# Kernel tuning notes

Measured on AMD Instinct MI355X. Metric: run time of the kernel, lower is better.

## Reference

```python
import jax, jax.numpy as jnp
import numpy as np

NEG = -9e15
LN_EPS = 1e-5
ALPHA = 0.2  # LeakyReLU negative slope


def setup_inputs() -> dict:
    key = jax.random.key(0)
    ks = jax.random.split(key, 10)
    B, N, Din, H, F, L = 8, 512, 64, 8, 128, 2
    x = jax.random.normal(ks[0], (B, N, Din), dtype=jnp.float32)
    adj = jax.random.randint(ks[1], (B, N, N), 0, 2, dtype=jnp.int32)
    Wp = jax.random.normal(ks[2], (Din, F), dtype=jnp.float32) * 0.12
    bp = jnp.zeros((F,), dtype=jnp.float32)
    W_heads = jax.random.normal(ks[3], (L, H, F, F), dtype=jnp.float32) * 0.08
    a_heads = jax.random.normal(ks[4], (L, H, 2 * F), dtype=jnp.float32) * 0.08
    W_out = jax.random.normal(ks[5], (L, H * F, F), dtype=jnp.float32) * 0.03
    a_out = jax.random.normal(ks[6], (L, 2 * F), dtype=jnp.float32) * 0.08
    ln_g = jnp.ones((L, F), dtype=jnp.float32)
    ln_b = jnp.zeros((L, F), dtype=jnp.float32)
    return {"x": x, "adj": adj, "Wp": Wp, "bp": bp, "W_heads": W_heads,
            "a_heads": a_heads, "W_out": W_out, "a_out": a_out,
            "ln_g": ln_g, "ln_b": ln_b}


def _gat_heads(x, W, a, adj_mask):
    # x:[B,N,Fin]  W:[H,Fin,F]  a:[H,2F]  adj_mask:[B,N,N] bool
    h = jnp.einsum('bni,hio->bhno', x, W)          # [B,H,N,F]
    F = h.shape[-1]
    # a_input @ a == (h_i . a1) + (h_j . a2): split attention vector,
    # mathematically identical to the concat formulation.
    s1 = jnp.einsum('bhnf,hf->bhn', h, a[:, :F])   # source term
    s2 = jnp.einsum('bhnf,hf->bhn', h, a[:, F:])   # target term
    e = jax.nn.leaky_relu(s1[:, :, :, None] + s2[:, :, None, :], ALPHA)  # [B,H,N,N]
    att = jnp.where(adj_mask[:, None], e, NEG)
    att = jax.nn.softmax(att, axis=-1)
    return jnp.einsum('bhnm,bhmf->bhnf', att, h)   # [B,H,N,F]


def _gat_single(x, W, a, adj_mask):
    # out_att head (concat=False, no ELU)
    h = jnp.einsum('bni,io->bno', x, W)            # [B,N,F]
    F = h.shape[-1]
    s1 = h @ a[:F]                                  # [B,N]
    s2 = h @ a[F:]
    e = jax.nn.leaky_relu(s1[:, :, None] + s2[:, None, :], ALPHA)
    att = jnp.where(adj_mask, e, NEG)
    att = jax.nn.softmax(att, axis=-1)
    return jnp.einsum('bnm,bmf->bnf', att, h)


def _layernorm(x, g, b):
    mu = jnp.mean(x, axis=-1, keepdims=True)
    var = jnp.var(x, axis=-1, keepdims=True)
    return (x - mu) * jax.lax.rsqrt(var + LN_EPS) * g + b


def reference(x, adj, Wp, bp, W_heads, a_heads, W_out, a_out, ln_g, ln_b):
    adj_mask = adj > 0                              # [B,N,N]
    L = W_heads.shape[0]
    B, N = x.shape[0], x.shape[1]
    # input projection (eval mode -> dropout is identity)
    h = jax.nn.relu(x @ Wp + bp)                    # [B,N,F]
    for i in range(L):
        residual = h
        heads = _gat_heads(h, W_heads[i], a_heads[i], adj_mask)      # [B,H,N,F]
        heads = jax.nn.elu(heads)                                     # concat=True -> ELU
        multi = jnp.transpose(heads, (0, 2, 1, 3)).reshape(B, N, -1)  # [B,N,H*F]
        out = _gat_single(multi, W_out[i], a_out[i], adj_mask)        # [B,N,F]
        h = _layernorm(out + residual, ln_g[i], ln_b[i])
        if i < L - 1:
            h = jax.nn.relu(h)
    return h
```

## Files before the change

kernel.cpp:

```cpp
#include <hip/hip_runtime.h>


constexpr int B = 8, N = 512, DIN = 64, H = 8, F = 128;
constexpr int BN = B * N;
constexpr float ALPHA_LR = 0.2f;
constexpr float EPS_LN = 1e-5f;
constexpr float FLOW = -3.0e38f;

typedef __attribute__((ext_vector_type(8))) short short8;
typedef __attribute__((ext_vector_type(4))) float f32x4;

__device__ __forceinline__ f32x4 mfma16(short8 a, short8 b, f32x4 c) {
  return __builtin_amdgcn_mfma_f32_16x16x32_bf16(a, b, c, 0, 0, 0);
}

__device__ __forceinline__ short f2bf(float f) {
  union { float f; unsigned u; } v;
  v.f = f;
  unsigned r = v.u + 0x7FFFu + ((v.u >> 16) & 1u);
  return (short)(r >> 16);
}

__global__ __launch_bounds__(256) void k_setup(
    const float* __restrict__ x, const int* __restrict__ adj,
    const float* __restrict__ Wp, const float* __restrict__ bp,
    const float* __restrict__ W_heads, const float* __restrict__ W_out,
    float* __restrict__ h, short* __restrict__ hb,
    unsigned long long* __restrict__ amask, short* __restrict__ WTh,
    short* __restrict__ WoT) {
  __shared__ float T[32][33];
  __shared__ float xr[2][64];
  int blk = blockIdx.x, tid = threadIdx.x;
  if (blk < 8192) {
    int w = blk * 4 + (tid >> 6);
    int lane = tid & 63;
    int v = adj[(size_t)w * 64 + lane];
    unsigned long long m = __ballot(v > 0);
    if (lane == 0) amask[w] = m;
  } else if (blk < 10240) {
    int rb = blk - 8192;
    int half = tid >> 7, f = tid & 127;
    int row = rb * 2 + half;
    if (f < 64) xr[half][f] = x[(size_t)row * DIN + f];
    __syncthreads();
    float acc = bp[f];
#pragma unroll
    for (int i = 0; i < DIN; i++) acc = fmaf(xr[half][i], Wp[i * F + f], acc);
    acc = fmaxf(acc, 0.f);
    h[(size_t)row * F + f] = acc;
    hb[(size_t)row * F + f] = f2bf(acc);
  } else {
    const float* in;
    short* out;
    int R, C, bx, by, bt;
    if (blk < 10496) {
      int i = blk - 10240;
      in = W_heads; out = WTh; R = 128; C = 128;
      bx = i & 3; by = (i >> 2) & 3; bt = i >> 4;
    } else {
      int i = blk - 10496;
      in = W_out; out = WoT; R = 1024; C = 128;
      bx = i & 3; by = (i >> 2) & 31; bt = i >> 7;
    }
    int c0 = bx * 32, r0 = by * 32;
    const float* ip = in + (size_t)bt * R * C;
    short* op = out + (size_t)bt * R * C;
    {
      int r = tid >> 3, c4 = (tid & 7) * 4;
      float4 v = *(const float4*)(ip + (size_t)(r0 + r) * C + c0 + c4);
      T[r][c4] = v.x; T[r][c4 + 1] = v.y; T[r][c4 + 2] = v.z; T[r][c4 + 3] = v.w;
    }
    __syncthreads();
    {
      int cr = tid >> 3, q = (tid & 7) * 4;
      short4 o;
      o.x = f2bf(T[q][cr]); o.y = f2bf(T[q + 1][cr]);
      o.z = f2bf(T[q + 2][cr]); o.w = f2bf(T[q + 3][cr]);
      *(short4*)(op + (size_t)(c0 + cr) * R + r0 + q) = o;
    }
  }
}

__global__ __launch_bounds__(256) void k_proj_heads_mfma(
    const short* __restrict__ WT, const short* __restrict__ hb,
    const float* __restrict__ ah_base, short* __restrict__ hhT,
    float* __restrict__ s1, float* __restrict__ s2) {
  int n0 = blockIdx.x * 128;
  int ft = blockIdx.y;
  int bh = blockIdx.z;
  int b = bh >> 3, hd = bh & 7;
  constexpr int LK = 136;
  __shared__ short As[64 * LK];
  __shared__ short Bs[128 * LK];
  int tid = threadIdx.x, lane = tid & 63, w = tid >> 6;
  {
    int r = tid >> 2, q = tid & 3;
    const uint4* g = (const uint4*)(WT + ((size_t)hd * F + ft * 64 + r) * F) + q * 4;
    uint4* lp = (uint4*)(As + r * LK) + q * 4;
    lp[0] = g[0]; lp[1] = g[1]; lp[2] = g[2]; lp[3] = g[3];
  }
  {
    int q = tid & 3;
    for (int r = tid >> 2; r < 128; r += 64) {
      const uint4* g = (const uint4*)(hb + ((size_t)(b * N + n0 + r)) * F) + q * 4;
      uint4* lp = (uint4*)(Bs + r * LK) + q * 4;
      lp[0] = g[0]; lp[1] = g[1]; lp[2] = g[2]; lp[3] = g[3];
    }
  }
  __syncthreads();
  int arow = lane & 15, koff = (lane >> 4) * 8;
  f32x4 acc[4][2] = {};
#pragma unroll
  for (int ks = 0; ks < 4; ks++) {
    short8 a[4], bb[2];
#pragma unroll
    for (int rt = 0; rt < 4; rt++)
      a[rt] = *(const short8*)(As + (rt * 16 + arow) * LK + ks * 32 + koff);
#pragma unroll
    for (int cj = 0; cj < 2; cj++)
      bb[cj] = *(const short8*)(Bs + ((2 * w + cj) * 16 + arow) * LK + ks * 32 + koff);
#pragma unroll
    for (int rt = 0; rt < 4; rt++)
#pragma unroll
      for (int cj = 0; cj < 2; cj++)
        acc[rt][cj] = mfma16(a[rt], bb[cj], acc[rt][cj]);
  }
  short* outp = hhT + (size_t)bh * F * N;
  int crow0 = (lane >> 4) * 4;
#pragma unroll
  for (int rt = 0; rt < 4; rt++)
#pragma unroll
    for (int cj = 0; cj < 2; cj++) {
      int fo = ft * 64 + rt * 16 + crow0;
      int n = n0 + (2 * w + cj) * 16 + arow;
#pragma unroll
      for (int r = 0; r < 4; r++)
        outp[(size_t)(fo + r) * N + n] = f2bf(acc[rt][cj][r]);
    }
  const float* ah = ah_base + (size_t)hd * 2 * F;
  float pa1[2] = {0.f, 0.f}, pa2[2] = {0.f, 0.f};
#pragma unroll
  for (int rt = 0; rt < 4; rt++) {
    int fo = ft * 64 + rt * 16 + crow0;
#pragma unroll
    for (int r = 0; r < 4; r++) {
      float a1v = ah[fo + r], a2v = ah[F + fo + r];
      pa1[0] = fmaf(a1v, acc[rt][0][r], pa1[0]);
      pa1[1] = fmaf(a1v, acc[rt][1][r], pa1[1]);
      pa2[0] = fmaf(a2v, acc[rt][0][r], pa2[0]);
      pa2[1] = fmaf(a2v, acc[rt][1][r], pa2[1]);
    }
  }
#pragma unroll
  for (int cj = 0; cj < 2; cj++) {
    float v1 = pa1[cj], v2 = pa2[cj];
    v1 += __shfl_xor(v1, 16); v1 += __shfl_xor(v1, 32);
    v2 += __shfl_xor(v2, 16); v2 += __shfl_xor(v2, 32);
    if (lane < 16) {
      int n = n0 + (2 * w + cj) * 16 + lane;
      atomicAdd(&s1[(size_t)bh * N + n], v1);
      atomicAdd(&s2[(size_t)bh * N + n], v2);
    }
  }
}

__global__ __launch_bounds__(256) void k_proj_out_mfma(
    const short* __restrict__ WoT, const short* __restrict__ multi,
    const float* __restrict__ ao, short* __restrict__ hsT,
    float* __restrict__ s1, float* __restrict__ s2) {
  int ft = blockIdx.x, nt = blockIdx.y, b = blockIdx.z;
  constexpr int LK = 136;
  __shared__ short As[32 * LK];
  __shared__ short Bs[64 * LK];
  int tid = threadIdx.x, lane = tid & 63, w = tid >> 6;
  int arow = lane & 15, koff = (lane >> 4) * 8;
  const int KT = H * F;
  f32x4 acc[2] = {};
  for (int k0 = 0; k0 < KT; k0 += 128) {
    __syncthreads();
    {
      int r = tid >> 3, e = tid & 7;
      const uint4* gp = (const uint4*)(WoT + (size_t)(ft * 32 + r) * KT + k0) + e * 2;
      uint4* lp = (uint4*)(As + r * LK) + e * 2;
      lp[0] = gp[0]; lp[1] = gp[1];
    }
    {
      int r = tid >> 2, q = tid & 3;
      const uint4* gp =
          (const uint4*)(multi + (size_t)(b * N + nt * 64 + r) * KT + k0) + q * 4;
      uint4* lp = (uint4*)(Bs + r * LK) + q * 4;
      lp[0] = gp[0]; lp[1] = gp[1]; lp[2] = gp[2]; lp[3] = gp[3];
    }
    __syncthreads();
#pragma unroll
    for (int ks = 0; ks < 4; ks++) {
      short8 b0 = *(const short8*)(Bs + (w * 16 + arow) * LK + ks * 32 + koff);
      short8 a0 = *(const short8*)(As + arow * LK + ks * 32 + koff);
      short8 a1 = *(const short8*)(As + (16 + arow) * LK + ks * 32 + koff);
      acc[0] = mfma16(a0, b0, acc[0]);
      acc[1] = mfma16(a1, b0, acc[1]);
    }
  }
  int crow0 = (lane >> 4) * 4;
  short* op = hsT + (size_t)b * F * N;
#pragma unroll
  for (int rt = 0; rt < 2; rt++)
#pragma unroll
    for (int r = 0; r < 4; r++)
      op[(size_t)(ft * 32 + rt * 16 + crow0 + r) * N + nt * 64 + w * 16 + arow] =
          f2bf(acc[rt][r]);
  float pa1 = 0.f, pa2 = 0.f;
#pragma unroll
  for (int rt = 0; rt < 2; rt++) {
    int fo = ft * 32 + rt * 16 + crow0;
#pragma unroll
    for (int r = 0; r < 4; r++) {
      pa1 = fmaf(ao[fo + r], acc[rt][r], pa1);
      pa2 = fmaf(ao[F + fo + r], acc[rt][r], pa2);
    }
  }
  pa1 += __shfl_xor(pa1, 16); pa1 += __shfl_xor(pa1, 32);
  pa2 += __shfl_xor(pa2, 16); pa2 += __shfl_xor(pa2, 32);
  if (lane < 16) {
    int n = nt * 64 + w * 16 + lane;
    atomicAdd(&s1[(size_t)b * N + n], pa1);
    atomicAdd(&s2[(size_t)b * N + n], pa2);
  }
}

__global__ __launch_bounds__(256) void k_attn_heads3(
    const short* __restrict__ VT, const float* __restrict__ s1g,
    const float* __restrict__ s2g, const unsigned long long* __restrict__ amask,
    short* __restrict__ multi) {
  int n0 = blockIdx.x * 64;
  int hd = blockIdx.y, b = blockIdx.z;
  int bh = b * H + hd;
  constexpr int LVK = 136;
  __shared__ short Vs[128 * LVK];
  __shared__ short Pf[16 * 64 * 8];
  __shared__ float s2all[512];
  __shared__ float s1r[64], mrow[64], linv[64];
  __shared__ float red[64][4];

  int tid = threadIdx.x, lane = tid & 63, w = tid >> 6;
  s2all[tid] = s2g[(size_t)bh * N + tid];
  s2all[tid + 256] = s2g[(size_t)bh * N + tid + 256];
  if (tid < 64) s1r[tid] = s1g[(size_t)bh * N + n0 + tid];
  __syncthreads();
  {
    const unsigned long long* mq = amask + ((size_t)(b * N + n0 + lane)) * 8;
    float mx = FLOW;
#pragma unroll
    for (int j = 0; j < 2; j++) {
      unsigned long long mb = mq[w * 2 + j];
      int base = w * 128 + j * 64;
      unsigned lo = (unsigned)mb, hi = (unsigned)(mb >> 32);
#pragma unroll
      for (int k = 0; k < 32; k++) {
        mx = ((lo >> k) & 1u) ? fmaxf(mx, s2all[base + k]) : mx;
        mx = ((hi >> k) & 1u) ? fmaxf(mx, s2all[base + 32 + k]) : mx;
      }
    }
    red[lane][w] = mx;
  }
  __syncthreads();
  if (tid < 64) {
    float m2 = fmaxf(fmaxf(red[tid][0], red[tid][1]),
                     fmaxf(red[tid][2], red[tid][3]));
    float xm = s1r[tid] + m2;
    mrow[tid] = xm > 0.f ? xm : ALPHA_LR * xm;
  }
  float lp = 0.f;
  int arow = lane & 15, koff = (lane >> 4) * 8;
  f32x4 acc[4][2] = {};
  const short* Vg = VT + (size_t)bh * F * N;
  const unsigned long long* mp = amask + ((size_t)(b * N + n0 + lane)) * 8;
  for (int mc = 0; mc < 4; mc++) {
    int m0 = mc * 128;
    __syncthreads();
    {
      int fr = tid >> 1, hf = tid & 1;
      const uint4* g4 = (const uint4*)(Vg + (size_t)fr * N + m0 + hf * 64);
      uint4* l4 = (uint4*)(Vs + fr * LVK + hf * 64);
#pragma unroll
      for (int k = 0; k < 8; k++) l4[k] = g4[k];
    }
    {
      float s1v = s1r[lane], mr = mrow[lane];
      unsigned bits = (unsigned)(mp[mc * 2 + (w >> 1)] >> ((w & 1) * 32));
      short* pbase = Pf + (((lane >> 4) * 4 + w) * 64) * 8;
#pragma unroll
      for (int q = 0; q < 4; q++) {
        short8 pk;
#pragma unroll
        for (int j = 0; j < 8; j++) {
          float xv = s1v + s2all[m0 + w * 32 + q * 8 + j];
          xv = xv > 0.f ? xv : ALPHA_LR * xv;
          float p = __expf(xv - mr);
          p = ((bits >> (q * 8 + j)) & 1u) ? p : 0.f;
          lp += p;
          pk[j] = f2bf(p);
        }
        *(short8*)(pbase + ((q << 4) | (lane & 15)) * 8) = pk;
      }
    }
    __syncthreads();
#pragma unroll
    for (int ks = 0; ks < 4; ks++) {
      short8 a[4];
#pragma unroll
      for (int rt = 0; rt < 4; rt++)
        a[rt] = *(const short8*)(Pf + ((rt * 4 + ks) * 64 + lane) * 8);
#pragma unroll
      for (int cj = 0; cj < 2; cj++) {
        short8 bb = *(const short8*)(Vs + ((w * 2 + cj) * 16 + arow) * LVK +
                                     ks * 32 + koff);
#pragma unroll
        for (int rt = 0; rt < 4; rt++)
          acc[rt][cj] = mfma16(a[rt], bb, acc[rt][cj]);
      }
    }
  }
  __syncthreads();
  red[lane][w] = lp;
  __syncthreads();
  if (tid < 64)
    linv[tid] = 1.f / (red[tid][0] + red[tid][1] + red[tid][2] + red[tid][3]);
  __syncthreads();
  int crow0 = (lane >> 4) * 4;
#pragma unroll
  for (int rt = 0; rt < 4; rt++)
#pragma unroll
    for (int cj = 0; cj < 2; cj++) {
      int fcol = (w * 2 + cj) * 16 + arow;
#pragma unroll
      for (int rr = 0; rr < 4; rr++) {
        int nrow = rt * 16 + crow0 + rr;
        float v = acc[rt][cj][rr] * linv[nrow];
        v = v > 0.f ? v : __expf(v) - 1.f;
        multi[((size_t)(b * N + n0 + nrow)) * (H * F) + hd * F + fcol] = f2bf(v);
      }
    }
}

template <int LAST>
__global__ __launch_bounds__(256) void k_attn_single3(
    const short* __restrict__ VT, const float* __restrict__ s1g,
    const float* __restrict__ s2g, const unsigned long long* __restrict__ amask,
    const float* __restrict__ resid, const float* __restrict__ lng,
    const float* __restrict__ lnb, float* __restrict__ hout,
    short* __restrict__ hbout, float* __restrict__ dout) {
  int n0 = blockIdx.x * 16;
  int b = blockIdx.y;
  constexpr int LVK = 136;
  __shared__ short Vs[128 * LVK];
  __shared__ short Pf[4 * 64 * 8];
  __shared__ float s2all[512];
  __shared__ float Ot[16][132];
  __shared__ float redS[16][16], redQ[16][16];
  __shared__ float s1r[16], mrow[16], linv[16], muA[16], rsA[16];

  int tid = threadIdx.x, lane = tid & 63, w = tid >> 6;
  s2all[tid] = s2g[(size_t)b * N + tid];
  s2all[tid + 256] = s2g[(size_t)b * N + tid + 256];
  if (tid < 16) s1r[tid] = s1g[(size_t)b * N + n0 + tid];
  __syncthreads();
  {
    int r = tid & 15, seg = tid >> 4;
    unsigned long long mb = amask[((size_t)(b * N + n0 + r)) * 8 + (seg >> 1)];
    unsigned bits = (unsigned)(mb >> ((seg & 1) * 32));
    float mx = FLOW;
#pragma unroll
    for (int k = 0; k < 32; k++)
      mx = ((bits >> k) & 1u) ? fmaxf(mx, s2all[seg * 32 + k]) : mx;
    redS[r][seg] = mx;
  }
  __syncthreads();
  if (tid < 16) {
    float m2 = FLOW;
#pragma unroll
    for (int k = 0; k < 16; k++) m2 = fmaxf(m2, redS[tid][k]);
    float xm = s1r[tid] + m2;
    mrow[tid] = xm > 0.f ? xm : ALPHA_LR * xm;
  }
  float lp = 0.f;
  int arow = lane & 15, koff = (lane >> 4) * 8;
  int pr = tid & 15, pq = (tid >> 4) & 3;
  f32x4 acc[2] = {};
  const short* Vg = VT + (size_t)b * F * N;
  const unsigned long long* mp = amask + ((size_t)(b * N + n0 + pr)) * 8;
  for (int mc = 0; mc < 4; mc++) {
    int m0 = mc * 128;
    __syncthreads();
    {
      int fr = tid >> 1, hf = tid & 1;
      const uint4* g4 = (const uint4*)(Vg + (size_t)fr * N + m0 + hf * 64);
      uint4* l4 = (uint4*)(Vs + fr * LVK + hf * 64);
#pragma unroll
      for (int k = 0; k < 8; k++) l4[k] = g4[k];
    }
    {
      float s1v = s1r[pr], mr = mrow[pr];
      unsigned bits = (unsigned)(mp[mc * 2 + (w >> 1)] >> ((w & 1) * 32));
      short8 pk;
#pragma unroll
      for (int j = 0; j < 8; j++) {
        float xv = s1v + s2all[m0 + w * 32 + pq * 8 + j];
        xv = xv > 0.f ? xv : ALPHA_LR * xv;
        float p = __expf(xv - mr);
        p = ((bits >> (pq * 8 + j)) & 1u) ? p : 0.f;
        lp += p;
        pk[j] = f2bf(p);
      }
      *(short8*)(Pf + (w * 64 + ((pq << 4) | pr)) * 8) = pk;
    }
    __syncthreads();
#pragma unroll
    for (int ks = 0; ks < 4; ks++) {
      short8 a = *(const short8*)(Pf + (ks * 64 + lane) * 8);
#pragma unroll
      for (int cj = 0; cj < 2; cj++) {
        short8 bb = *(const short8*)(Vs + ((w * 2 + cj) * 16 + arow) * LVK +
                                     ks * 32 + koff);
        acc[cj] = mfma16(a, bb, acc[cj]);
      }
    }
  }
  __syncthreads();
  redS[pr][tid >> 4] = lp;
  __syncthreads();
  if (tid < 16) {
    float l = 0.f;
#pragma unroll
    for (int k = 0; k < 16; k++) l += redS[tid][k];
    linv[tid] = 1.f / l;
  }
  __syncthreads();
  int crow0 = (lane >> 4) * 4;
#pragma unroll
  for (int cj = 0; cj < 2; cj++) {
    int fcol = (w * 2 + cj) * 16 + arow;
#pragma unroll
    for (int rr = 0; rr < 4; rr++) {
      int row = crow0 + rr;
      Ot[row][fcol] = acc[cj][rr] * linv[row];
    }
  }
  __syncthreads();
  int r2 = tid >> 4, f8 = (tid & 15) * 8;
  size_t gbase = ((size_t)(b * N + n0 + r2)) * F + f8;
  float v[8];
  float s = 0.f, sq = 0.f;
#pragma unroll
  for (int j = 0; j < 8; j++) {
    float t = Ot[r2][f8 + j] + resid[gbase + j];
    v[j] = t;
    s += t;
    sq = fmaf(t, t, sq);
  }
  redS[r2][tid & 15] = s;
  redQ[r2][tid & 15] = sq;
  __syncthreads();
  if (tid < 16) {
    float ss = 0.f, qq = 0.f;
#pragma unroll
    for (int k = 0; k < 16; k++) { ss += redS[tid][k]; qq += redQ[tid][k]; }
    float mu = ss * (1.f / F);
    muA[tid] = mu;
    rsA[tid] = rsqrtf(qq * (1.f / F) - mu * mu + EPS_LN);
  }
  __syncthreads();
  float mu = muA[r2], rs = rsA[r2];
#pragma unroll
  for (int j = 0; j < 8; j++) {
    float y = (v[j] - mu) * rs * lng[f8 + j] + lnb[f8 + j];
    if (LAST) {
      dout[gbase + j] = y;
    } else {
      y = fmaxf(y, 0.f);
      hout[gbase + j] = y;
      hbout[gbase + j] = f2bf(y);
    }
  }
}

extern "C" void kernel_launch(void* const* d_in, const int* in_sizes, int n_in,
                              void* d_out, int out_size, void* d_ws,
                              size_t ws_size, hipStream_t stream) {
  const float* x = (const float*)d_in[0];
  const int* adj = (const int*)d_in[1];
  const float* Wp = (const float*)d_in[2];
  const float* bp = (const float*)d_in[3];
  const float* W_heads = (const float*)d_in[4];
  const float* a_heads = (const float*)d_in[5];
  const float* W_out = (const float*)d_in[6];
  const float* a_out = (const float*)d_in[7];
  const float* ln_g = (const float*)d_in[8];
  const float* ln_b = (const float*)d_in[9];

  char* p = (char*)d_ws;
  auto alloc = [&](size_t bytes) {
    char* r = p;
    p += (bytes + 255) & ~(size_t)255;
    return r;
  };
  float* sA = (float*)alloc((size_t)2 * 73728 * 4);
  short* WTh = (short*)alloc((size_t)2 * H * F * F * 2);
  short* WoT = (short*)alloc((size_t)2 * H * F * F * 2);
  unsigned long long* amask = (unsigned long long*)alloc((size_t)BN * 8 * 8);
  float* h = (float*)alloc((size_t)BN * F * 4);
  short* hb = (short*)alloc((size_t)BN * F * 2);
  short* hhT = (short*)alloc((size_t)B * H * F * N * 2);
  short* multi = (short*)alloc((size_t)BN * H * F * 2);
  short* hsT = (short*)alloc((size_t)B * F * N * 2);

  hipMemsetAsync(sA, 0, (size_t)2 * 73728 * 4, stream);
  k_setup<<<dim3(10752), 256, 0, stream>>>(x, adj, Wp, bp, W_heads, W_out, h,
                                           hb, amask, WTh, WoT);
  for (int l = 0; l < 2; l++) {
    float* s1h = sA + (size_t)l * 73728;
    float* s2h = s1h + 32768;
    float* s1o = s2h + 32768;
    float* s2o = s1o + 4096;
    k_proj_heads_mfma<<<dim3(4, 2, 64), 256, 0, stream>>>(
        WTh + (size_t)l * H * F * F, hb, a_heads + (size_t)l * H * 2 * F, hhT,
        s1h, s2h);
    k_attn_heads3<<<dim3(8, 8, 8), 256, 0, stream>>>(hhT, s1h, s2h, amask,
                                                     multi);
    k_proj_out_mfma<<<dim3(4, 8, 8), 256, 0, stream>>>(
        WoT + (size_t)l * F * H * F, multi, a_out + (size_t)l * 2 * F, hsT, s1o,
        s2o);
    if (l == 0)
      k_attn_single3<0><<<dim3(32, 8), 256, 0, stream>>>(
          hsT, s1o, s2o, amask, h, ln_g, ln_b, h, hb, nullptr);
    else
      k_attn_single3<1><<<dim3(32, 8), 256, 0, stream>>>(
          hsT, s1o, s2o, amask, h, ln_g + F, ln_b + F, nullptr, nullptr,
          (float*)d_out);
  }
}
```

Measured before the change: 189.7 us.

## Fuse all GAT stages into one cooperative persistent kernel with grid syncs

```diff
diff --git a/kernel.cpp b/kernel.cpp
--- a/kernel.cpp
+++ b/kernel.cpp
@@ -1,5 +1,8 @@
 #include <hip/hip_runtime.h>
-
+#include <hip/hip_cooperative_groups.h>
+
+
+namespace cg = cooperative_groups;
 
 constexpr int B = 8, N = 512, DIN = 64, H = 8, F = 128;
 constexpr int BN = B * N;
@@ -21,89 +24,114 @@
   return (short)(r >> 16);
 }
 
-__global__ __launch_bounds__(256) void k_setup(
-    const float* __restrict__ x, const int* __restrict__ adj,
-    const float* __restrict__ Wp, const float* __restrict__ bp,
-    const float* __restrict__ W_heads, const float* __restrict__ W_out,
-    float* __restrict__ h, short* __restrict__ hb,
-    unsigned long long* __restrict__ amask, short* __restrict__ WTh,
-    short* __restrict__ WoT) {
-  __shared__ float T[32][33];
-  __shared__ float xr[2][64];
-  int blk = blockIdx.x, tid = threadIdx.x;
-  if (blk < 8192) {
-    int w = blk * 4 + (tid >> 6);
-    int lane = tid & 63;
-    int v = adj[(size_t)w * 64 + lane];
-    unsigned long long m = __ballot(v > 0);
-    if (lane == 0) amask[w] = m;
-  } else if (blk < 10240) {
-    int rb = blk - 8192;
+struct KParams {
+  const float* x; const int* adj; const float* Wp; const float* bp;
+  const float* W_heads; const float* a_heads; const float* W_out;
+  const float* a_out; const float* ln_g; const float* ln_b;
+  float* h; short* hb; unsigned long long* amask; short* WTh; short* WoT;
+  short* hhT; short* multi; short* hsT; float* sA; float* dout;
+};
+
+struct SM_PH { short As[64 * 136]; short Bs[128 * 136]; };
+struct SM_AH {
+  short Vs[128 * 136]; short Pf[16 * 64 * 8]; float s2all[512];
+  float s1r[64]; float mrow[64]; float linv[64]; float red[64][4];
+};
+struct SM_PO { short As[32 * 136]; short Bs[32 * 136]; };
+struct SM_AS {
+  short Vs[128 * 136]; short Pf[4 * 64 * 8]; float s2all[512];
+  float Ot[16][132]; float redS[16][16]; float redQ[16][16];
+  float s1r[16]; float mrow[16]; float linv[16]; float muA[16]; float rsA[16];
+};
+struct SM_SU { float T[32][33]; float xr[2][64]; };
+
+__device__ __forceinline__ void st_setup(const KParams& P, int bid, int tid,
+                                         char* smraw) {
+  for (int i = tid; i < 288; i += 256) P.sA[(size_t)bid * 288 + i] = 0.f;
+  {
+    int lane = tid & 63, wv = tid >> 6;
+    int v[16];
+#pragma unroll
+    for (int j = 0; j < 16; j++) {
+      int w = (bid + j * 512) * 4 + wv;
+      v[j] = P.adj[(size_t)w * 64 + lane];
+    }
+#pragma unroll
+    for (int j = 0; j < 16; j++) {
+      int w = (bid + j * 512) * 4 + wv;
+      unsigned long long m = __ballot(v[j] > 0);
+      if (lane == 0) P.amask[w] = m;
+    }
+  }
+  {
+    SM_SU* s = (SM_SU*)smraw;
     int half = tid >> 7, f = tid & 127;
-    int row = rb * 2 + half;
-    if (f < 64) xr[half][f] = x[(size_t)row * DIN + f];
-    __syncthreads();
-    float acc = bp[f];
-#pragma unroll
-    for (int i = 0; i < DIN; i++) acc = fmaf(xr[half][i], Wp[i * F + f], acc);
-    acc = fmaxf(acc, 0.f);
-    h[(size_t)row * F + f] = acc;
-    hb[(size_t)row * F + f] = f2bf(acc);
-  } else {
-    const float* in;
-    short* out;
-    int R, C, bx, by, bt;
-    if (blk < 10496) {
-      int i = blk - 10240;
-      in = W_heads; out = WTh; R = 128; C = 128;
-      bx = i & 3; by = (i >> 2) & 3; bt = i >> 4;
+    for (int u = bid; u < 2048; u += 512) {
+      int row = u * 2 + half;
+      __syncthreads();
+      if (f < 64) s->xr[half][f] = P.x[(size_t)row * DIN + f];
+      __syncthreads();
+      float acc = P.bp[f];
+#pragma unroll
+      for (int i = 0; i < DIN; i++)
+        acc = fmaf(s->xr[half][i], P.Wp[i * F + f], acc);
+      acc = fmaxf(acc, 0.f);
+      P.h[(size_t)row * F + f] = acc;
+      P.hb[(size_t)row * F + f] = f2bf(acc);
+    }
+  }
+  {
+    SM_SU* s = (SM_SU*)smraw;
+    const float* in; short* out; int R, C, bx, by, bt;
+    if (bid < 256) {
+      in = P.W_heads; out = P.WTh; R = 128; C = 128;
+      bx = bid & 3; by = (bid >> 2) & 3; bt = bid >> 4;
     } else {
-      int i = blk - 10496;
-      in = W_out; out = WoT; R = 1024; C = 128;
+      int i = bid - 256;
+      in = P.W_out; out = P.WoT; R = 1024; C = 128;
       bx = i & 3; by = (i >> 2) & 31; bt = i >> 7;
     }
     int c0 = bx * 32, r0 = by * 32;
     const float* ip = in + (size_t)bt * R * C;
     short* op = out + (size_t)bt * R * C;
+    __syncthreads();
     {
       int r = tid >> 3, c4 = (tid & 7) * 4;
       float4 v = *(const float4*)(ip + (size_t)(r0 + r) * C + c0 + c4);
-      T[r][c4] = v.x; T[r][c4 + 1] = v.y; T[r][c4 + 2] = v.z; T[r][c4 + 3] = v.w;
+      s->T[r][c4] = v.x; s->T[r][c4 + 1] = v.y;
+      s->T[r][c4 + 2] = v.z; s->T[r][c4 + 3] = v.w;
     }
     __syncthreads();
     {
       int cr = tid >> 3, q = (tid & 7) * 4;
       short4 o;
-      o.x = f2bf(T[q][cr]); o.y = f2bf(T[q + 1][cr]);
-      o.z = f2bf(T[q + 2][cr]); o.w = f2bf(T[q + 3][cr]);
+      o.x = f2bf(s->T[q][cr]); o.y = f2bf(s->T[q + 1][cr]);
+      o.z = f2bf(s->T[q + 2][cr]); o.w = f2bf(s->T[q + 3][cr]);
       *(short4*)(op + (size_t)(c0 + cr) * R + r0 + q) = o;
     }
   }
 }
 
-__global__ __launch_bounds__(256) void k_proj_heads_mfma(
-    const short* __restrict__ WT, const short* __restrict__ hb,
-    const float* __restrict__ ah_base, short* __restrict__ hhT,
-    float* __restrict__ s1, float* __restrict__ s2) {
-  int n0 = blockIdx.x * 128;
-  int ft = blockIdx.y;
-  int bh = blockIdx.z;
+__device__ __forceinline__ void st_proj_heads(
+    const KParams& P, const short* WT, const float* ah_base, float* s1,
+    float* s2, int bid, int tid, char* smraw) {
+  SM_PH* sm = (SM_PH*)smraw;
+  int nt = bid & 3, ft = (bid >> 2) & 1, bh = bid >> 3;
   int b = bh >> 3, hd = bh & 7;
+  int n0 = nt * 128;
   constexpr int LK = 136;
-  __shared__ short As[64 * LK];
-  __shared__ short Bs[128 * LK];
-  int tid = threadIdx.x, lane = tid & 63, w = tid >> 6;
+  int lane = tid & 63, w = tid >> 6;
   {
     int r = tid >> 2, q = tid & 3;
     const uint4* g = (const uint4*)(WT + ((size_t)hd * F + ft * 64 + r) * F) + q * 4;
-    uint4* lp = (uint4*)(As + r * LK) + q * 4;
+    uint4* lp = (uint4*)(sm->As + r * LK) + q * 4;
     lp[0] = g[0]; lp[1] = g[1]; lp[2] = g[2]; lp[3] = g[3];
   }
   {
     int q = tid & 3;
     for (int r = tid >> 2; r < 128; r += 64) {
-      const uint4* g = (const uint4*)(hb + ((size_t)(b * N + n0 + r)) * F) + q * 4;
-      uint4* lp = (uint4*)(Bs + r * LK) + q * 4;
+      const uint4* g = (const uint4*)(P.hb + ((size_t)(b * N + n0 + r)) * F) + q * 4;
+      uint4* lp = (uint4*)(sm->Bs + r * LK) + q * 4;
       lp[0] = g[0]; lp[1] = g[1]; lp[2] = g[2]; lp[3] = g[3];
     }
   }
@@ -115,17 +143,18 @@
     short8 a[4], bb[2];
 #pragma unroll
     for (int rt = 0; rt < 4; rt++)
-      a[rt] = *(const short8*)(As + (rt * 16 + arow) * LK + ks * 32 + koff);
+      a[rt] = *(const short8*)(sm->As + (rt * 16 + arow) * LK + ks * 32 + koff);
 #pragma unroll
     for (int cj = 0; cj < 2; cj++)
-      bb[cj] = *(const short8*)(Bs + ((2 * w + cj) * 16 + arow) * LK + ks * 32 + koff);
+      bb[cj] = *(const short8*)(sm->Bs + ((2 * w + cj) * 16 + arow) * LK +
+                                ks * 32 + koff);
 #pragma unroll
     for (int rt = 0; rt < 4; rt++)
 #pragma unroll
       for (int cj = 0; cj < 2; cj++)
         acc[rt][cj] = mfma16(a[rt], bb[cj], acc[rt][cj]);
   }
-  short* outp = hhT + (size_t)bh * F * N;
+  short* outp = P.hhT + (size_t)bh * F * N;
   int crow0 = (lane >> 4) * 4;
 #pragma unroll
   for (int rt = 0; rt < 4; rt++)
@@ -164,91 +193,20 @@
   }
 }
 
-__global__ __launch_bounds__(256) void k_proj_out_mfma(
-    const short* __restrict__ WoT, const short* __restrict__ multi,
-    const float* __restrict__ ao, short* __restrict__ hsT,
-    float* __restrict__ s1, float* __restrict__ s2) {
-  int ft = blockIdx.x, nt = blockIdx.y, b = blockIdx.z;
-  constexpr int LK = 136;
-  __shared__ short As[32 * LK];
-  __shared__ short Bs[64 * LK];
-  int tid = threadIdx.x, lane = tid & 63, w = tid >> 6;
-  int arow = lane & 15, koff = (lane >> 4) * 8;
-  const int KT = H * F;
-  f32x4 acc[2] = {};
-  for (int k0 = 0; k0 < KT; k0 += 128) {
-    __syncthreads();
-    {
-      int r = tid >> 3, e = tid & 7;
-      const uint4* gp = (const uint4*)(WoT + (size_t)(ft * 32 + r) * KT + k0) + e * 2;
-      uint4* lp = (uint4*)(As + r * LK) + e * 2;
-      lp[0] = gp[0]; lp[1] = gp[1];
-    }
-    {
-      int r = tid >> 2, q = tid & 3;
-      const uint4* gp =
-          (const uint4*)(multi + (size_t)(b * N + nt * 64 + r) * KT + k0) + q * 4;
-      uint4* lp = (uint4*)(Bs + r * LK) + q * 4;
-      lp[0] = gp[0]; lp[1] = gp[1]; lp[2] = gp[2]; lp[3] = gp[3];
-    }
-    __syncthreads();
-#pragma unroll
-    for (int ks = 0; ks < 4; ks++) {
-      short8 b0 = *(const short8*)(Bs + (w * 16 + arow) * LK + ks * 32 + koff);
-      short8 a0 = *(const short8*)(As + arow * LK + ks * 32 + koff);
-      short8 a1 = *(const short8*)(As + (16 + arow) * LK + ks * 32 + koff);
-      acc[0] = mfma16(a0, b0, acc[0]);
-      acc[1] = mfma16(a1, b0, acc[1]);
-    }
-  }
-  int crow0 = (lane >> 4) * 4;
-  short* op = hsT + (size_t)b * F * N;
-#pragma unroll
-  for (int rt = 0; rt < 2; rt++)
-#pragma unroll
-    for (int r = 0; r < 4; r++)
-      op[(size_t)(ft * 32 + rt * 16 + crow0 + r) * N + nt * 64 + w * 16 + arow] =
-          f2bf(acc[rt][r]);
-  float pa1 = 0.f, pa2 = 0.f;
-#pragma unroll
-  for (int rt = 0; rt < 2; rt++) {
-    int fo = ft * 32 + rt * 16 + crow0;
-#pragma unroll
-    for (int r = 0; r < 4; r++) {
-      pa1 = fmaf(ao[fo + r], acc[rt][r], pa1);
-      pa2 = fmaf(ao[F + fo + r], acc[rt][r], pa2);
-    }
-  }
-  pa1 += __shfl_xor(pa1, 16); pa1 += __shfl_xor(pa1, 32);
-  pa2 += __shfl_xor(pa2, 16); pa2 += __shfl_xor(pa2, 32);
-  if (lane < 16) {
-    int n = nt * 64 + w * 16 + lane;
-    atomicAdd(&s1[(size_t)b * N + n], pa1);
-    atomicAdd(&s2[(size_t)b * N + n], pa2);
-  }
-}
-
-__global__ __launch_bounds__(256) void k_attn_heads3(
-    const short* __restrict__ VT, const float* __restrict__ s1g,
-    const float* __restrict__ s2g, const unsigned long long* __restrict__ amask,
-    short* __restrict__ multi) {
-  int n0 = blockIdx.x * 64;
-  int hd = blockIdx.y, b = blockIdx.z;
-  int bh = b * H + hd;
+__device__ __forceinline__ void st_attn_heads(
+    const KParams& P, const float* s1g, const float* s2g, int bid, int tid,
+    char* smraw) {
+  SM_AH* sm = (SM_AH*)smraw;
+  int nt = bid & 7, hd = (bid >> 3) & 7, b = bid >> 6;
+  int n0 = nt * 64, bh = b * H + hd;
   constexpr int LVK = 136;
-  __shared__ short Vs[128 * LVK];
-  __shared__ short Pf[16 * 64 * 8];
-  __shared__ float s2all[512];
-  __shared__ float s1r[64], mrow[64], linv[64];
-  __shared__ float red[64][4];
-
-  int tid = threadIdx.x, lane = tid & 63, w = tid >> 6;
-  s2all[tid] = s2g[(size_t)bh * N + tid];
-  s2all[tid + 256] = s2g[(size_t)bh * N + tid + 256];
-  if (tid < 64) s1r[tid] = s1g[(size_t)bh * N + n0 + tid];
-  __syncthreads();
-  {
-    const unsigned long long* mq = amask + ((size_t)(b * N + n0 + lane)) * 8;
+  int lane = tid & 63, w = tid >> 6;
+  sm->s2all[tid] = s2g[(size_t)bh * N + tid];
+  sm->s2all[tid + 256] = s2g[(size_t)bh * N + tid + 256];
+  if (tid < 64) sm->s1r[tid] = s1g[(size_t)bh * N + n0 + tid];
+  __syncthreads();
+  {
+    const unsigned long long* mq = P.amask + ((size_t)(b * N + n0 + lane)) * 8;
     float mx = FLOW;
 #pragma unroll
     for (int j = 0; j < 2; j++) {
@@ -257,44 +215,44 @@
       unsigned lo = (unsigned)mb, hi = (unsigned)(mb >> 32);
 #pragma unroll
       for (int k = 0; k < 32; k++) {
-        mx = ((lo >> k) & 1u) ? fmaxf(mx, s2all[base + k]) : mx;
-        mx = ((hi >> k) & 1u) ? fmaxf(mx, s2all[base + 32 + k]) : mx;
+        mx = ((lo >> k) & 1u) ? fmaxf(mx, sm->s2all[base + k]) : mx;
+        mx = ((hi >> k) & 1u) ? fmaxf(mx, sm->s2all[base + 32 + k]) : mx;
       }
     }
-    red[lane][w] = mx;
+    sm->red[lane][w] = mx;
   }
   __syncthreads();
   if (tid < 64) {
-    float m2 = fmaxf(fmaxf(red[tid][0], red[tid][1]),
-                     fmaxf(red[tid][2], red[tid][3]));
-    float xm = s1r[tid] + m2;
-    mrow[tid] = xm > 0.f ? xm : ALPHA_LR * xm;
+    float m2 = fmaxf(fmaxf(sm->red[tid][0], sm->red[tid][1]),
+                     fmaxf(sm->red[tid][2], sm->red[tid][3]));
+    float xm = sm->s1r[tid] + m2;
+    sm->mrow[tid] = xm > 0.f ? xm : ALPHA_LR * xm;
   }
   float lp = 0.f;
   int arow = lane & 15, koff = (lane >> 4) * 8;
   f32x4 acc[4][2] = {};
-  const short* Vg = VT + (size_t)bh * F * N;
-  const unsigned long long* mp = amask + ((size_t)(b * N + n0 + lane)) * 8;
+  const short* Vg = P.hhT + (size_t)bh * F * N;
+  const unsigned long long* mp = P.amask + ((size_t)(b * N + n0 + lane)) * 8;
   for (int mc = 0; mc < 4; mc++) {
     int m0 = mc * 128;
     __syncthreads();
     {
       int fr = tid >> 1, hf = tid & 1;
       const uint4* g4 = (const uint4*)(Vg + (size_t)fr * N + m0 + hf * 64);
-      uint4* l4 = (uint4*)(Vs + fr * LVK + hf * 64);
+      uint4* l4 = (uint4*)(sm->Vs + fr * LVK + hf * 64);
 #pragma unroll
       for (int k = 0; k < 8; k++) l4[k] = g4[k];
     }
     {
-      float s1v = s1r[lane], mr = mrow[lane];
+      float s1v = sm->s1r[lane], mr = sm->mrow[lane];
       unsigned bits = (unsigned)(mp[mc * 2 + (w >> 1)] >> ((w & 1) * 32));
-      short* pbase = Pf + (((lane >> 4) * 4 + w) * 64) * 8;
+      short* pbase = sm->Pf + (((lane >> 4) * 4 + w) * 64) * 8;
 #pragma unroll
       for (int q = 0; q < 4; q++) {
         short8 pk;
 #pragma unroll
         for (int j = 0; j < 8; j++) {
-          float xv = s1v + s2all[m0 + w * 32 + q * 8 + j];
+          float xv = s1v + sm->s2all[m0 + w * 32 + q * 8 + j];
           xv = xv > 0.f ? xv : ALPHA_LR * xv;
           float p = __expf(xv - mr);
           p = ((bits >> (q * 8 + j)) & 1u) ? p : 0.f;
@@ -310,10 +268,10 @@
       short8 a[4];
 #pragma unroll
       for (int rt = 0; rt < 4; rt++)
-        a[rt] = *(const short8*)(Pf + ((rt * 4 + ks) * 64 + lane) * 8);
+        a[rt] = *(const short8*)(sm->Pf + ((rt * 4 + ks) * 64 + lane) * 8);
 #pragma unroll
       for (int cj = 0; cj < 2; cj++) {
-        short8 bb = *(const short8*)(Vs + ((w * 2 + cj) * 16 + arow) * LVK +
+        short8 bb = *(const short8*)(sm->Vs + ((w * 2 + cj) * 16 + arow) * LVK +
                                      ks * 32 + koff);
 #pragma unroll
         for (int rt = 0; rt < 4; rt++)
@@ -322,10 +280,11 @@
     }
   }
   __syncthreads();
-  red[lane][w] = lp;
+  sm->red[lane][w] = lp;
   __syncthreads();
   if (tid < 64)
-    linv[tid] = 1.f / (red[tid][0] + red[tid][1] + red[tid][2] + red[tid][3]);
+    sm->linv[tid] = 1.f / (sm->red[tid][0] + sm->red[tid][1] +
+                           sm->red[tid][2] + sm->red[tid][3]);
   __syncthreads();
   int crow0 = (lane >> 4) * 4;
 #pragma unroll
@@ -336,104 +295,155 @@
 #pragma unroll
       for (int rr = 0; rr < 4; rr++) {
         int nrow = rt * 16 + crow0 + rr;
-        float v = acc[rt][cj][rr] * linv[nrow];
+        float v = acc[rt][cj][rr] * sm->linv[nrow];
         v = v > 0.f ? v : __expf(v) - 1.f;
-        multi[((size_t)(b * N + n0 + nrow)) * (H * F) + hd * F + fcol] = f2bf(v);
+        P.multi[((size_t)(b * N + n0 + nrow)) * (H * F) + hd * F + fcol] =
+            f2bf(v);
       }
     }
 }
 
-template <int LAST>
-__global__ __launch_bounds__(256) void k_attn_single3(
-    const short* __restrict__ VT, const float* __restrict__ s1g,
-    const float* __restrict__ s2g, const unsigned long long* __restrict__ amask,
-    const float* __restrict__ resid, const float* __restrict__ lng,
-    const float* __restrict__ lnb, float* __restrict__ hout,
-    short* __restrict__ hbout, float* __restrict__ dout) {
-  int n0 = blockIdx.x * 16;
-  int b = blockIdx.y;
+__device__ __forceinline__ void st_proj_out(
+    const KParams& P, const short* WoT, const float* ao, float* s1, float* s2,
+    int bid, int tid, char* smraw) {
+  SM_PO* sm = (SM_PO*)smraw;
+  int ft = bid & 3, nt = (bid >> 2) & 15, b = bid >> 6;
+  int f0 = ft * 32, nb = nt * 32;
+  constexpr int LK = 136;
+  int lane = tid & 63, w = tid >> 6;
+  int rt = w & 1, ct = w >> 1;
+  int arow = lane & 15, koff = (lane >> 4) * 8;
+  const int KT = H * F;
+  f32x4 acc = {};
+  for (int k0 = 0; k0 < KT; k0 += 128) {
+    __syncthreads();
+    {
+      int r = tid >> 3, e = tid & 7;
+      const uint4* gp = (const uint4*)(WoT + (size_t)(f0 + r) * KT + k0) + e * 2;
+      uint4* lp = (uint4*)(sm->As + r * LK) + e * 2;
+      lp[0] = gp[0]; lp[1] = gp[1];
+    }
+    {
+      int r = tid >> 3, e = tid & 7;
+      const uint4* gp =
+          (const uint4*)(P.multi + (size_t)(b * N + nb + r) * KT + k0) + e * 2;
+      uint4* lp = (uint4*)(sm->Bs + r * LK) + e * 2;
+      lp[0] = gp[0]; lp[1] = gp[1];
+    }
+    __syncthreads();
+#pragma unroll
+    for (int ks = 0; ks < 4; ks++) {
+      short8 a = *(const short8*)(sm->As + (rt * 16 + arow) * LK + ks * 32 + koff);
+      short8 bb = *(const short8*)(sm->Bs + (ct * 16 + arow) * LK + ks * 32 + koff);
+      acc = mfma16(a, bb, acc);
+    }
+  }
+  int crow0 = (lane >> 4) * 4;
+  short* op = P.hsT + (size_t)b * F * N;
+#pragma unroll
+  for (int r = 0; r < 4; r++)
+    op[(size_t)(f0 + rt * 16 + crow0 + r) * N + nb + ct * 16 + arow] =
+        f2bf(acc[r]);
+  float pa1 = 0.f, pa2 = 0.f;
+  {
+    int fo = f0 + rt * 16 + crow0;
+#pragma unroll
+    for (int r = 0; r < 4; r++) {
+      pa1 = fmaf(ao[fo + r], acc[r], pa1);
+      pa2 = fmaf(ao[F + fo + r], acc[r], pa2);
+    }
+  }
+  pa1 += __shfl_xor(pa1, 16); pa1 += __shfl_xor(pa1, 32);
+  pa2 += __shfl_xor(pa2, 16); pa2 += __shfl_xor(pa2, 32);
+  if (lane < 16) {
+    int n = nb + ct * 16 + lane;
+    atomicAdd(&s1[(size_t)b * N + n], pa1);
+    atomicAdd(&s2[(size_t)b * N + n], pa2);
+  }
+}
+
+__device__ __forceinline__ void st_attn_single(
+    const KParams& P, const float* s1g, const float* s2g, const float* lng,
+    const float* lnb, int last, int bid, int tid, char* smraw) {
+  SM_AS* sm = (SM_AS*)smraw;
+  int nt = bid & 31, b = bid >> 5;
+  int n0 = nt * 16;
   constexpr int LVK = 136;
-  __shared__ short Vs[128 * LVK];
-  __shared__ short Pf[4 * 64 * 8];
-  __shared__ float s2all[512];
-  __shared__ float Ot[16][132];
-  __shared__ float redS[16][16], redQ[16][16];
-  __shared__ float s1r[16], mrow[16], linv[16], muA[16], rsA[16];
-
-  int tid = threadIdx.x, lane = tid & 63, w = tid >> 6;
-  s2all[tid] = s2g[(size_t)b * N + tid];
-  s2all[tid + 256] = s2g[(size_t)b * N + tid + 256];
-  if (tid < 16) s1r[tid] = s1g[(size_t)b * N + n0 + tid];
+  int lane = tid & 63, w = tid >> 6;
+  sm->s2all[tid] = s2g[(size_t)b * N + tid];
+  sm->s2all[tid + 256] = s2g[(size_t)b * N + tid + 256];
+  if (tid < 16) sm->s1r[tid] = s1g[(size_t)b * N + n0 + tid];
   __syncthreads();
   {
     int r = tid & 15, seg = tid >> 4;
-    unsigned long long mb = amask[((size_t)(b * N + n0 + r)) * 8 + (seg >> 1)];
+    unsigned long long mb =
+        P.amask[((size_t)(b * N + n0 + r)) * 8 + (seg >> 1)];
     unsigned bits = (unsigned)(mb >> ((seg & 1) * 32));
     float mx = FLOW;
 #pragma unroll
     for (int k = 0; k < 32; k++)
-      mx = ((bits >> k) & 1u) ? fmaxf(mx, s2all[seg * 32 + k]) : mx;
-    redS[r][seg] = mx;
+      mx = ((bits >> k) & 1u) ? fmaxf(mx, sm->s2all[seg * 32 + k]) : mx;
+    sm->redS[r][seg] = mx;
   }
   __syncthreads();
   if (tid < 16) {
     float m2 = FLOW;
 #pragma unroll
-    for (int k = 0; k < 16; k++) m2 = fmaxf(m2, redS[tid][k]);
-    float xm = s1r[tid] + m2;
-    mrow[tid] = xm > 0.f ? xm : ALPHA_LR * xm;
+    for (int k = 0; k < 16; k++) m2 = fmaxf(m2, sm->redS[tid][k]);
+    float xm = sm->s1r[tid] + m2;
+    sm->mrow[tid] = xm > 0.f ? xm : ALPHA_LR * xm;
   }
   float lp = 0.f;
   int arow = lane & 15, koff = (lane >> 4) * 8;
   int pr = tid & 15, pq = (tid >> 4) & 3;
   f32x4 acc[2] = {};
-  const short* Vg = VT + (size_t)b * F * N;
-  const unsigned long long* mp = amask + ((size_t)(b * N + n0 + pr)) * 8;
+  const short* Vg = P.hsT + (size_t)b * F * N;
+  const unsigned long long* mp = P.amask + ((size_t)(b * N + n0 + pr)) * 8;
   for (int mc = 0; mc < 4; mc++) {
     int m0 = mc * 128;
     __syncthreads();
     {
       int fr = tid >> 1, hf = tid & 1;
       const uint4* g4 = (const uint4*)(Vg + (size_t)fr * N + m0 + hf * 64);
-      uint4* l4 = (uint4*)(Vs + fr * LVK + hf * 64);
+      uint4* l4 = (uint4*)(sm->Vs + fr * LVK + hf * 64);
 #pragma unroll
       for (int k = 0; k < 8; k++) l4[k] = g4[k];
     }
     {
-      float s1v = s1r[pr], mr = mrow[pr];
+      float s1v = sm->s1r[pr], mr = sm->mrow[pr];
       unsigned bits = (unsigned)(mp[mc * 2 + (w >> 1)] >> ((w & 1) * 32));
       short8 pk;
 #pragma unroll
       for (int j = 0; j < 8; j++) {
-        float xv = s1v + s2all[m0 + w * 32 + pq * 8 + j];
+        float xv = s1v + sm->s2all[m0 + w * 32 + pq * 8 + j];
         xv = xv > 0.f ? xv : ALPHA_LR * xv;
         float p = __expf(xv - mr);
         p = ((bits >> (pq * 8 + j)) & 1u) ? p : 0.f;
         lp += p;
         pk[j] = f2bf(p);
       }
-      *(short8*)(Pf + (w * 64 + ((pq << 4) | pr)) * 8) = pk;
+      *(short8*)(sm->Pf + (w * 64 + ((pq << 4) | pr)) * 8) = pk;
     }
     __syncthreads();
 #pragma unroll
     for (int ks = 0; ks < 4; ks++) {
-      short8 a = *(const short8*)(Pf + (ks * 64 + lane) * 8);
+      short8 a = *(const short8*)(sm->Pf + (ks * 64 + lane) * 8);
 #pragma unroll
       for (int cj = 0; cj < 2; cj++) {
-        short8 bb = *(const short8*)(Vs + ((w * 2 + cj) * 16 + arow) * LVK +
+        short8 bb = *(const short8*)(sm->Vs + ((w * 2 + cj) * 16 + arow) * LVK +
                                      ks * 32 + koff);
         acc[cj] = mfma16(a, bb, acc[cj]);
       }
     }
   }
   __syncthreads();
-  redS[pr][tid >> 4] = lp;
+  sm->redS[pr][tid >> 4] = lp;
   __syncthreads();
   if (tid < 16) {
     float l = 0.f;
 #pragma unroll
-    for (int k = 0; k < 16; k++) l += redS[tid][k];
-    linv[tid] = 1.f / l;
+    for (int k = 0; k < 16; k++) l += sm->redS[tid][k];
+    sm->linv[tid] = 1.f / l;
   }
   __syncthreads();
   int crow0 = (lane >> 4) * 4;
@@ -443,7 +453,7 @@
 #pragma unroll
     for (int rr = 0; rr < 4; rr++) {
       int row = crow0 + rr;
-      Ot[row][fcol] = acc[cj][rr] * linv[row];
+      sm->Ot[row][fcol] = acc[cj][rr] * sm->linv[row];
     }
   }
   __syncthreads();
@@ -453,89 +463,144 @@
   float s = 0.f, sq = 0.f;
 #pragma unroll
   for (int j = 0; j < 8; j++) {
-    float t = Ot[r2][f8 + j] + resid[gbase + j];
+    float t = sm->Ot[r2][f8 + j] + P.h[gbase + j];
     v[j] = t;
     s += t;
     sq = fmaf(t, t, sq);
   }
-  redS[r2][tid & 15] = s;
-  redQ[r2][tid & 15] = sq;
+  sm->redS[r2][tid & 15] = s;
+  sm->redQ[r2][tid & 15] = sq;
   __syncthreads();
   if (tid < 16) {
     float ss = 0.f, qq = 0.f;
 #pragma unroll
-    for (int k = 0; k < 16; k++) { ss += redS[tid][k]; qq += redQ[tid][k]; }
+    for (int k = 0; k < 16; k++) { ss += sm->redS[tid][k]; qq += sm->redQ[tid][k]; }
     float mu = ss * (1.f / F);
-    muA[tid] = mu;
-    rsA[tid] = rsqrtf(qq * (1.f / F) - mu * mu + EPS_LN);
-  }
-  __syncthreads();
-  float mu = muA[r2], rs = rsA[r2];
+    sm->muA[tid] = mu;
+    sm->rsA[tid] = rsqrtf(qq * (1.f / F) - mu * mu + EPS_LN);
+  }
+  __syncthreads();
+  float mu = sm->muA[r2], rs = sm->rsA[r2];
 #pragma unroll
   for (int j = 0; j < 8; j++) {
     float y = (v[j] - mu) * rs * lng[f8 + j] + lnb[f8 + j];
-    if (LAST) {
-      dout[gbase + j] = y;
+    if (last) {
+      P.dout[gbase + j] = y;
     } else {
       y = fmaxf(y, 0.f);
-      hout[gbase + j] = y;
-      hbout[gbase + j] = f2bf(y);
-    }
-  }
+      P.h[gbase + j] = y;
+      P.hb[gbase + j] = f2bf(y);
+    }
+  }
+}
+
+__global__ __launch_bounds__(256, 2) void k_mega(KParams P) {
+  cg::grid_group grid = cg::this_grid();
+  __shared__ alignas(16) char smem[sizeof(SM_AH)];
+  int bid = blockIdx.x, tid = threadIdx.x;
+
+  st_setup(P, bid, tid, smem);
+  __threadfence(); grid.sync();
+
+  for (int l = 0; l < 2; l++) {
+    const short* WTh_l = P.WTh + (size_t)l * H * F * F;
+    const float* ah_l = P.a_heads + (size_t)l * H * 2 * F;
+    const short* WoT_l = P.WoT + (size_t)l * H * F * F;
+    const float* ao_l = P.a_out + (size_t)l * 2 * F;
+    float* s1h = P.sA + (size_t)l * 73728;
+    float* s2h = s1h + 32768;
+    float* s1o = s2h + 32768;
+    float* s2o = s1o + 4096;
+
+    st_proj_heads(P, WTh_l, ah_l, s1h, s2h, bid, tid, smem);
+    __threadfence(); grid.sync();
+    st_attn_heads(P, s1h, s2h, bid, tid, smem);
+    __threadfence(); grid.sync();
+    st_proj_out(P, WoT_l, ao_l, s1o, s2o, bid, tid, smem);
+    __threadfence(); grid.sync();
+    if (bid < 256)
+      st_attn_single(P, s1o, s2o, P.ln_g + (size_t)l * F,
+                     P.ln_b + (size_t)l * F, l == 1, bid, tid, smem);
+    if (l == 0) { __threadfence(); grid.sync(); }
+  }
+}
+
+__global__ __launch_bounds__(256) void g_setup(KParams P) {
+  __shared__ alignas(16) char smem[sizeof(SM_SU)];
+  st_setup(P, blockIdx.x, threadIdx.x, smem);
+}
+__global__ __launch_bounds__(256) void g_proj_heads(KParams P, int l) {
+  __shared__ alignas(16) char smem[sizeof(SM_PH)];
+  float* s1h = P.sA + (size_t)l * 73728;
+  st_proj_heads(P, P.WTh + (size_t)l * H * F * F,
+                P.a_heads + (size_t)l * H * 2 * F, s1h, s1h + 32768,
+                blockIdx.x, threadIdx.x, smem);
+}
+__global__ __launch_bounds__(256) void g_attn_heads(KParams P, int l) {
+  __shared__ alignas(16) char smem[sizeof(SM_AH)];
+  float* s1h = P.sA + (size_t)l * 73728;
+  st_attn_heads(P, s1h, s1h + 32768, blockIdx.x, threadIdx.x, smem);
+}
+__global__ __launch_bounds__(256) void g_proj_out(KParams P, int l) {
+  __shared__ alignas(16) char smem[sizeof(SM_PO)];
+  float* s1o = P.sA + (size_t)l * 73728 + 65536;
+  st_proj_out(P, P.WoT + (size_t)l * H * F * F,
+              P.a_out + (size_t)l * 2 * F, s1o, s1o + 4096, blockIdx.x,
+              threadIdx.x, smem);
+}
+__global__ __launch_bounds__(256) void g_attn_single(KParams P, int l) {
+  __shared__ alignas(16) char smem[sizeof(SM_AS)];
+  float* s1o = P.sA + (size_t)l * 73728 + 65536;
+  st_attn_single(P, s1o, s1o + 4096, P.ln_g + (size_t)l * F,
+                 P.ln_b + (size_t)l * F, l == 1, blockIdx.x, threadIdx.x,
+                 smem);
 }
 
 extern "C" void kernel_launch(void* const* d_in, const int* in_sizes, int n_in,
                               void* d_out, int out_size, void* d_ws,
                               size_t ws_size, hipStream_t stream) {
-  const float* x = (const float*)d_in[0];
-  const int* adj = (const int*)d_in[1];
-  const float* Wp = (const float*)d_in[2];
-  const float* bp = (const float*)d_in[3];
-  const float* W_heads = (const float*)d_in[4];
-  const float* a_heads = (const float*)d_in[5];
-  const float* W_out = (const float*)d_in[6];
-  const float* a_out = (const float*)d_in[7];
-  const float* ln_g = (const float*)d_in[8];
-  const float* ln_b = (const float*)d_in[9];
-
   char* p = (char*)d_ws;
   auto alloc = [&](size_t bytes) {
     char* r = p;
     p += (bytes + 255) & ~(size_t)255;
     return r;
   };
-  float* sA = (float*)alloc((size_t)2 * 73728 * 4);
-  short* WTh = (short*)alloc((size_t)2 * H * F * F * 2);
-  short* WoT = (short*)alloc((size_t)2 * H * F * F * 2);
-  unsigned long long* amask = (unsigned long long*)alloc((size_t)BN * 8 * 8);
-  float* h = (float*)alloc((size_t)BN * F * 4);
-  short* hb = (short*)alloc((size_t)BN * F * 2);
-  short* hhT = (short*)alloc((size_t)B * H * F * N * 2);
-  short* multi = (short*)alloc((size_t)BN * H * F * 2);
-  short* hsT = (short*)alloc((size_t)B * F * N * 2);
-
-  hipMemsetAsync(sA, 0, (size_t)2 * 73728 * 4, stream);
-  k_setup<<<dim3(10752), 256, 0, stream>>>(x, adj, Wp, bp, W_heads, W_out, h,
-                                           hb, amask, WTh, WoT);
+  KParams P;
+  P.x = (const float*)d_in[0];
+  P.adj = (const int*)d_in[1];
+  P.Wp = (const float*)d_in[2];
+  P.bp = (const float*)d_in[3];
+  P.W_heads = (const float*)d_in[4];
+  P.a_heads = (const float*)d_in[5];
+  P.W_out = (const float*)d_in[6];
+  P.a_out = (const float*)d_in[7];
+  P.ln_g = (const float*)d_in[8];
+  P.ln_b = (const float*)d_in[9];
+  P.sA = (float*)alloc((size_t)2 * 73728 * 4);
+  P.WTh = (short*)alloc((size_t)2 * H * F * F * 2);
+  P.WoT = (short*)alloc((size_t)2 * H * F * F * 2);
+  P.amask = (unsigned long long*)alloc((size_t)BN * 8 * 8);
+  P.h = (float*)alloc((size_t)BN * F * 4);
+  P.hb = (short*)alloc((size_t)BN * F * 2);
+  P.hhT = (short*)alloc((size_t)B * H * F * N * 2);
+  P.multi = (short*)alloc((size_t)BN * H * F * 2);
+  P.hsT = (short*)alloc((size_t)B * F * N * 2);
+  P.dout = (float*)d_out;
+
+  int occ = 0;
+  (void)hipOccupancyMaxActiveBlocksPerMultiprocessor(&occ, k_mega, 256, 0);
+  if (occ >= 2) {
+    void* kargs[] = {&P};
+    hipError_t e = hipLaunchCooperativeKernel((void*)k_mega, dim3(512),
+                                              dim3(256), kargs, 0, stream);
+    if (e == hipSuccess) return;
+    (void)hipGetLastError();
+  }
+  g_setup<<<512, 256, 0, stream>>>(P);
   for (int l = 0; l < 2; l++) {
-    float* s1h = sA + (size_t)l * 73728;
-    float* s2h = s1h + 32768;
-    float* s1o = s2h + 32768;
-    float* s2o = s1o + 4096;
-    k_proj_heads_mfma<<<dim3(4, 2, 64), 256, 0, stream>>>(
-        WTh + (size_t)l * H * F * F, hb, a_heads + (size_t)l * H * 2 * F, hhT,
-        s1h, s2h);
-    k_attn_heads3<<<dim3(8, 8, 8), 256, 0, stream>>>(hhT, s1h, s2h, amask,
-                                                     multi);
-    k_proj_out_mfma<<<dim3(4, 8, 8), 256, 0, stream>>>(
-        WoT + (size_t)l * F * H * F, multi, a_out + (size_t)l * 2 * F, hsT, s1o,
-        s2o);
-    if (l == 0)
-      k_attn_single3<0><<<dim3(32, 8), 256, 0, stream>>>(
-          hsT, s1o, s2o, amask, h, ln_g, ln_b, h, hb, nullptr);
-    else
-      k_attn_single3<1><<<dim3(32, 8), 256, 0, stream>>>(
-          hsT, s1o, s2o, amask, h, ln_g + F, ln_b + F, nullptr, nullptr,
-          (float*)d_out);
-  }
-}
+    g_proj_heads<<<512, 256, 0, stream>>>(P, l);
+    g_attn_heads<<<512, 256, 0, stream>>>(P, l);
+    g_proj_out<<<512, 256, 0, stream>>>(P, l);
+    g_attn_single<<<256, 256, 0, stream>>>(P, l);
+  }
+}
```

New measurement: 195.6 us. 3.1% more time.
